# Optimization experiments

Measured on AMD Instinct MI355X. Metric: run time of the kernel, lower is better.

The kernel has to match this reference:

```python
import jax, jax.numpy as jnp
import numpy as np

N_NODES = 50000
N_EDGES = 800000
IN_DIM = 128
HID = 64
ZDIM = 64
N_GRAPHS = 64


def gcn_conv(x, W, b, src, dst, n):
    # PyG GCNConv: add self-loops, symmetric deg^-1/2 normalization,
    # linear transform then gather-scatter aggregation.
    h = x @ W  # [N, out]
    loops = jnp.arange(n, dtype=src.dtype)
    s = jnp.concatenate([src, loops])
    d = jnp.concatenate([dst, loops])
    deg = jnp.zeros((n,), h.dtype).at[d].add(1.0)  # includes self-loops -> >=1
    dinv = jax.lax.rsqrt(deg)
    norm = dinv[s] * dinv[d]  # [E+N]
    msg = h[s] * norm[:, None]  # gather [E+N, out]
    out = jnp.zeros_like(h).at[d].add(msg)  # scatter-add
    return out + b


def mean_pool(h, batch, num_graphs):
    sums = jax.ops.segment_sum(h, batch, num_segments=num_graphs)
    cnt = jax.ops.segment_sum(jnp.ones((h.shape[0],), h.dtype), batch,
                              num_segments=num_graphs)
    return sums / jnp.maximum(cnt, 1.0)[:, None]


def setup_inputs() -> dict:
    key = jax.random.key(0)
    ks = jax.random.split(key, 9)
    x = jax.random.normal(ks[0], (N_NODES, IN_DIM), jnp.float32)
    edge_index = jax.random.randint(ks[1], (2, N_EDGES), 0, N_NODES, jnp.int64 if jax.config.jax_enable_x64 else jnp.int32)
    batch = jnp.sort(jax.random.randint(ks[2], (N_NODES,), 0, N_GRAPHS))
    s1 = 1.0 / np.sqrt(IN_DIM)
    s2 = 1.0 / np.sqrt(HID)
    W1 = jax.random.uniform(ks[3], (IN_DIM, HID), jnp.float32, -s1, s1)
    b1 = jnp.zeros((HID,), jnp.float32)
    Wmu = jax.random.uniform(ks[4], (HID, ZDIM), jnp.float32, -s2, s2)
    bmu = jnp.zeros((ZDIM,), jnp.float32)
    Wsig = jax.random.uniform(ks[5], (HID, ZDIM), jnp.float32, -s2, s2)
    bsig = jnp.zeros((ZDIM,), jnp.float32)
    return {"x": x, "edge_index": edge_index, "batch": batch,
            "num_graphs": N_GRAPHS, "W1": W1, "b1": b1,
            "Wmu": Wmu, "bmu": bmu, "Wsig": Wsig, "bsig": bsig}


def reference(x, edge_index, batch, num_graphs, W1, b1, Wmu, bmu, Wsig, bsig):
    src, dst = edge_index[0], edge_index[1]
    n = x.shape[0]
    h = jax.nn.elu(gcn_conv(x, W1, b1, src, dst, n))
    z_mu = mean_pool(jax.nn.elu(gcn_conv(h, Wmu, bmu, src, dst, n)), batch, num_graphs)
    z_sigma = mean_pool(jax.nn.elu(gcn_conv(h, Wsig, bsig, src, dst, n)), batch, num_graphs)
    return (z_mu, z_sigma)
```

## Files before the change

kernel.cpp:

```cpp
#include <hip/hip_runtime.h>
#include <hip/hip_fp16.h>


#define IN_DIM 128
#define HID 64
#define ZDIM 64
#define N_GRAPHS 64
#define SCAN_B 1024

typedef _Float16 half8 __attribute__((ext_vector_type(8)));
typedef float f32x4 __attribute__((ext_vector_type(4)));

__device__ __forceinline__ float elu1(float x) {
    return x > 0.f ? x : expm1f(x);
}

#define ACC8(RV, MV) do { \
    const __half2* _hp = (const __half2*)&(RV); \
    float2 _f0 = __half22float2(_hp[0]); \
    float2 _f1 = __half22float2(_hp[1]); \
    float2 _f2 = __half22float2(_hp[2]); \
    float2 _f3 = __half22float2(_hp[3]); \
    acc[0] = fmaf((MV), _f0.x, acc[0]); \
    acc[1] = fmaf((MV), _f0.y, acc[1]); \
    acc[2] = fmaf((MV), _f1.x, acc[2]); \
    acc[3] = fmaf((MV), _f1.y, acc[3]); \
    acc[4] = fmaf((MV), _f2.x, acc[4]); \
    acc[5] = fmaf((MV), _f2.y, acc[5]); \
    acc[6] = fmaf((MV), _f3.x, acc[6]); \
    acc[7] = fmaf((MV), _f3.y, acc[7]); \
  } while (0)

__global__ __launch_bounds__(256) void k_count_wfrag(const int* __restrict__ dst,
                                                     int* __restrict__ kc,
                                                     int* __restrict__ rank, int E,
                                                     const float* __restrict__ W1,
                                                     const float* __restrict__ Wmu,
                                                     const float* __restrict__ Wsig,
                                                     __half* __restrict__ F1,
                                                     __half* __restrict__ Fmu,
                                                     __half* __restrict__ Fsig,
                                                     int cntBlocks) {
    if ((int)blockIdx.x < cntBlocks) {
        int e = (blockIdx.x * 256 + threadIdx.x) * 2;
        if (e + 1 < E) {
            int2 d2 = *(const int2*)&dst[e];
            int r0 = atomicAdd(&kc[d2.x], 1);
            int r1 = atomicAdd(&kc[d2.y], 1);
            *(int2*)&rank[e] = make_int2(r0, r1);
        } else if (e < E) {
            rank[e] = atomicAdd(&kc[dst[e]], 1);
        }
        return;
    }
    int e = (blockIdx.x - cntBlocks) * 256 + threadIdx.x;
    if (e < 8192) {
        int j = e & 7, l = (e >> 3) & 63, ct = (e >> 9) & 3, ks = e >> 11;
        F1[e] = __float2half(W1[(ks * 32 + ((l >> 4) & 3) * 8 + j) * 64 + ct * 16 + (l & 15)]);
    }
    if (e < 4096) {
        int j = e & 7, l = (e >> 3) & 63, ct = (e >> 9) & 3, ks = e >> 11;
        int widx = (ks * 32 + ((l >> 4) & 3) * 8 + j) * 64 + ct * 16 + (l & 15);
        Fmu[e] = __float2half(Wmu[widx]);
        Fsig[e] = __float2half(Wsig[widx]);
    }
}

__global__ __launch_bounds__(SCAN_B) void k_scan1(const int* __restrict__ kc,
                                                  int* __restrict__ bsum, int n) {
    __shared__ int wpart[16];
    int tid = threadIdx.x, lane = tid & 63, w = tid >> 6;
    int i = blockIdx.x * SCAN_B + tid;
    int v = (i < n) ? kc[i] : 0;
#pragma unroll
    for (int d = 1; d < 64; d <<= 1) v += __shfl_xor(v, d, 64);
    if (lane == 0) wpart[w] = v;
    __syncthreads();
    if (tid < 16) {
        int t = wpart[tid];
#pragma unroll
        for (int d = 1; d < 16; d <<= 1) t += __shfl_xor(t, d, 64);
        if (tid == 0) bsum[blockIdx.x] = t;
    }
}

__global__ __launch_bounds__(SCAN_B) void k_scan3(const int* __restrict__ kc,
                                                  const int* __restrict__ bsum,
                                                  int* __restrict__ offs,
                                                  float* __restrict__ dinv,
                                                  int n, int nb) {
    __shared__ int wsum[16];
    __shared__ int sbase;
    int tid = threadIdx.x, lane = tid & 63, w = tid >> 6;
    if (tid < 64) {
        int v = (tid < nb) ? bsum[tid] : 0;
        int s = v;
#pragma unroll
        for (int d = 1; d < 64; d <<= 1) {
            int u = __shfl_up(s, d, 64);
            if (tid >= d) s += u;
        }
        if (tid == blockIdx.x) sbase = s - v;
    }
    int i = blockIdx.x * SCAN_B + tid;
    int v = (i < n) ? kc[i] : 0;
    int s = v;
#pragma unroll
    for (int d = 1; d < 64; d <<= 1) {
        int u = __shfl_up(s, d, 64);
        if (lane >= d) s += u;
    }
    if (lane == 63) wsum[w] = s;
    __syncthreads();
    if (tid < 16) {
        int t = wsum[tid];
#pragma unroll
        for (int d = 1; d < 16; d <<= 1) {
            int u = __shfl_up(t, d, 64);
            if (tid >= d) t += u;
        }
        wsum[tid] = t;
    }
    __syncthreads();
    int base = sbase + ((w == 0) ? 0 : wsum[w - 1]);
    if (i < n) {
        offs[i + 1] = base + s;
        dinv[i] = 1.0f / sqrtf(1.0f + (float)v);
        if (i == 0) offs[0] = 0;
    }
}

__global__ __launch_bounds__(256) void k_fill_mm1(const int* __restrict__ src,
                                                  const int* __restrict__ dst,
                                                  const int* __restrict__ rank,
                                                  const int* __restrict__ offs,
                                                  int* __restrict__ csr, int E,
                                                  const float* __restrict__ x,
                                                  const __half* __restrict__ F1,
                                                  const float* __restrict__ dinv,
                                                  __half* __restrict__ ts1h, int n,
                                                  int fillBlocks) {
    if ((int)blockIdx.x < fillBlocks) {
        int e = (blockIdx.x * 256 + threadIdx.x) * 2;
        if (e + 1 < E) {
            int2 s2 = *(const int2*)&src[e];
            int2 d2 = *(const int2*)&dst[e];
            int2 r2 = *(const int2*)&rank[e];
            csr[offs[d2.x] + r2.x] = s2.x;
            csr[offs[d2.y] + r2.y] = s2.y;
        } else if (e < E) {
            csr[offs[dst[e]] + rank[e]] = src[e];
        }
        return;
    }
    int bid = blockIdx.x - fillBlocks;
    int l = threadIdx.x & 63;
    int wave = threadIdx.x >> 6;
    int m0 = bid * 64 + wave * 16;
    int row_a = m0 + (l & 15);
    if (row_a >= n) row_a = n - 1;
    int kg = l >> 4;

    f32x4 acc0 = {0.f, 0.f, 0.f, 0.f};
    f32x4 acc1 = acc0, acc2 = acc0, acc3 = acc0;

    const float* xr = x + (size_t)row_a * IN_DIM + kg * 8;
#pragma unroll
    for (int ks = 0; ks < 4; ++ks) {
        float4 xa = *(const float4*)(xr + ks * 32);
        float4 xb = *(const float4*)(xr + ks * 32 + 4);
        half8 a;
        a[0] = (_Float16)xa.x; a[1] = (_Float16)xa.y;
        a[2] = (_Float16)xa.z; a[3] = (_Float16)xa.w;
        a[4] = (_Float16)xb.x; a[5] = (_Float16)xb.y;
        a[6] = (_Float16)xb.z; a[7] = (_Float16)xb.w;
        const __half* fb = F1 + ((size_t)(ks * 4) * 64 + l) * 8;
        half8 b0 = *(const half8*)(fb);
        half8 b1 = *(const half8*)(fb + 512);
        half8 b2 = *(const half8*)(fb + 1024);
        half8 b3 = *(const half8*)(fb + 1536);
        acc0 = __builtin_amdgcn_mfma_f32_16x16x32_f16(a, b0, acc0, 0, 0, 0);
        acc1 = __builtin_amdgcn_mfma_f32_16x16x32_f16(a, b1, acc1, 0, 0, 0);
        acc2 = __builtin_amdgcn_mfma_f32_16x16x32_f16(a, b2, acc2, 0, 0, 0);
        acc3 = __builtin_amdgcn_mfma_f32_16x16x32_f16(a, b3, acc3, 0, 0, 0);
    }
    int col = l & 15;
#pragma unroll
    for (int r = 0; r < 4; ++r) {
        int row = m0 + kg * 4 + r;
        if (row < n) {
            float di = dinv[row];
            __half* p = &ts1h[(size_t)row * 64 + col];
            p[0]  = __float2half(acc0[r] * di);
            p[16] = __float2half(acc1[r] * di);
            p[32] = __float2half(acc2[r] * di);
            p[48] = __float2half(acc3[r] * di);
        }
    }
}

__global__ __launch_bounds__(256) void k_gather_hh(const int* __restrict__ off,
                                                   const int* __restrict__ csr,
                                                   const float* __restrict__ dinv,
                                                   const __half* __restrict__ ts,
                                                   const float* __restrict__ b1,
                                                   __half* __restrict__ hh, int n) {
    int node = blockIdx.x * 4 + (threadIdx.x >> 6);
    if (node >= n) return;
    int lane = threadIdx.x & 63;
    int g = lane >> 3, sub = lane & 7;
    int s0 = off[node], s1 = off[node + 1];
    float acc[8];
#pragma unroll
    for (int j = 0; j < 8; ++j) acc[j] = 0.f;

    if (s1 > s0) {
        int last = s1 - 1;
        int p0 = s0 + g, p1 = p0 + 8, p2 = p0 + 16, p3 = p0 + 24;
        int i0 = csr[p0 < s1 ? p0 : last];
        int i1 = csr[p1 < s1 ? p1 : last];
        int i2 = csr[p2 < s1 ? p2 : last];
        int i3 = csr[p3 < s1 ? p3 : last];
        float4 r0 = *(const float4*)&ts[(size_t)i0 * 64 + sub * 8];
        float4 r1 = *(const float4*)&ts[(size_t)i1 * 64 + sub * 8];
        float4 r2 = *(const float4*)&ts[(size_t)i2 * 64 + sub * 8];
        float4 r3 = *(const float4*)&ts[(size_t)i3 * 64 + sub * 8];
        float m0 = (p0 < s1) ? 1.f : 0.f;
        float m1 = (p1 < s1) ? 1.f : 0.f;
        float m2 = (p2 < s1) ? 1.f : 0.f;
        float m3 = (p3 < s1) ? 1.f : 0.f;
        ACC8(r0, m0);
        ACC8(r1, m1);
        ACC8(r2, m2);
        ACC8(r3, m3);
        for (int k = s0 + 32 + g; k < s1; k += 8) {
            int iv = csr[k];
            float4 rv = *(const float4*)&ts[(size_t)iv * 64 + sub * 8];
            ACC8(rv, 1.f);
        }
    }

#pragma unroll
    for (int j = 0; j < 8; ++j) {
        acc[j] += __shfl_xor(acc[j], 8, 64);
        acc[j] += __shfl_xor(acc[j], 16, 64);
        acc[j] += __shfl_xor(acc[j], 32, 64);
    }

    if (g == 0) {
        float4 sr = *(const float4*)&ts[(size_t)node * 64 + sub * 8];
        const __half2* sh = (const __half2*)&sr;
        float di = dinv[node];
        const float4* b4 = (const float4*)b1;
        float4 ba = b4[sub * 2], bb = b4[sub * 2 + 1];
        float2 f0 = __half22float2(sh[0]);
        float2 f1 = __half22float2(sh[1]);
        float2 f2 = __half22float2(sh[2]);
        float2 f3 = __half22float2(sh[3]);
        float e0 = elu1((acc[0] + f0.x) * di + ba.x) * di;
        float e1 = elu1((acc[1] + f0.y) * di + ba.y) * di;
        float e2 = elu1((acc[2] + f1.x) * di + ba.z) * di;
        float e3 = elu1((acc[3] + f1.y) * di + ba.w) * di;
        float e4 = elu1((acc[4] + f2.x) * di + bb.x) * di;
        float e5 = elu1((acc[5] + f2.y) * di + bb.y) * di;
        float e6 = elu1((acc[6] + f3.x) * di + bb.z) * di;
        float e7 = elu1((acc[7] + f3.y) * di + bb.w) * di;
        float4 outv;
        __half2* op = (__half2*)&outv;
        op[0] = __floats2half2_rn(e0, e1);
        op[1] = __floats2half2_rn(e2, e3);
        op[2] = __floats2half2_rn(e4, e5);
        op[3] = __floats2half2_rn(e6, e7);
        *(float4*)&hh[(size_t)node * 64 + sub * 8] = outv;
    }
}

__global__ __launch_bounds__(256) void k_gather_g(const int* __restrict__ off,
                                                  const int* __restrict__ csr,
                                                  const float* __restrict__ dinv,
                                                  const __half* __restrict__ hh,
                                                  __half* __restrict__ gh2, int n) {
    int node = blockIdx.x * 4 + (threadIdx.x >> 6);
    if (node >= n) return;
    int lane = threadIdx.x & 63;
    int g = lane >> 3, sub = lane & 7;
    int s0 = off[node], s1 = off[node + 1];
    float acc[8];
#pragma unroll
    for (int j = 0; j < 8; ++j) acc[j] = 0.f;

    if (s1 > s0) {
        int last = s1 - 1;
        int p0 = s0 + g, p1 = p0 + 8, p2 = p0 + 16, p3 = p0 + 24;
        int i0 = csr[p0 < s1 ? p0 : last];
        int i1 = csr[p1 < s1 ? p1 : last];
        int i2 = csr[p2 < s1 ? p2 : last];
        int i3 = csr[p3 < s1 ? p3 : last];
        float4 r0 = *(const float4*)&hh[(size_t)i0 * 64 + sub * 8];
        float4 r1 = *(const float4*)&hh[(size_t)i1 * 64 + sub * 8];
        float4 r2 = *(const float4*)&hh[(size_t)i2 * 64 + sub * 8];
        float4 r3 = *(const float4*)&hh[(size_t)i3 * 64 + sub * 8];
        float m0 = (p0 < s1) ? 1.f : 0.f;
        float m1 = (p1 < s1) ? 1.f : 0.f;
        float m2 = (p2 < s1) ? 1.f : 0.f;
        float m3 = (p3 < s1) ? 1.f : 0.f;
        ACC8(r0, m0);
        ACC8(r1, m1);
        ACC8(r2, m2);
        ACC8(r3, m3);
        for (int k = s0 + 32 + g; k < s1; k += 8) {
            int iv = csr[k];
            float4 rv = *(const float4*)&hh[(size_t)iv * 64 + sub * 8];
            ACC8(rv, 1.f);
        }
    }

#pragma unroll
    for (int j = 0; j < 8; ++j) {
        acc[j] += __shfl_xor(acc[j], 8, 64);
        acc[j] += __shfl_xor(acc[j], 16, 64);
        acc[j] += __shfl_xor(acc[j], 32, 64);
    }

    if (g == 0) {
        float4 sr = *(const float4*)&hh[(size_t)node * 64 + sub * 8];
        const __half2* sh = (const __half2*)&sr;
        float di = dinv[node];
        float2 f0 = __half22float2(sh[0]);
        float2 f1 = __half22float2(sh[1]);
        float2 f2 = __half22float2(sh[2]);
        float2 f3 = __half22float2(sh[3]);
        float4 outv;
        __half2* op = (__half2*)&outv;
        op[0] = __floats2half2_rn((acc[0] + f0.x) * di, (acc[1] + f0.y) * di);
        op[1] = __floats2half2_rn((acc[2] + f1.x) * di, (acc[3] + f1.y) * di);
        op[2] = __floats2half2_rn((acc[4] + f2.x) * di, (acc[5] + f2.y) * di);
        op[3] = __floats2half2_rn((acc[6] + f3.x) * di, (acc[7] + f3.y) * di);
        *(float4*)&gh2[(size_t)node * 64 + sub * 8] = outv;
    }
}

__global__ __launch_bounds__(256) void k_mm_pool(const __half* __restrict__ gh2,
                                                 const __half* __restrict__ Fmu,
                                                 const __half* __restrict__ Fsig,
                                                 const float* __restrict__ bmu,
                                                 const float* __restrict__ bsig,
                                                 const int* __restrict__ batch,
                                                 float* __restrict__ sums, int n) {
    __shared__ float wc[64 * 132];
    __shared__ int bs[64];
    const int tid = threadIdx.x;
    int l = tid & 63, wave = tid >> 6;
    int m0 = blockIdx.x * 64;
    int row_a = m0 + wave * 16 + (l & 15);
    if (row_a >= n) row_a = n - 1;
    int kg = l >> 4;

    f32x4 am[4], as[4];
#pragma unroll
    for (int ct = 0; ct < 4; ++ct) {
        am[ct] = (f32x4){0.f, 0.f, 0.f, 0.f};
        as[ct] = (f32x4){0.f, 0.f, 0.f, 0.f};
    }

    const __half* gr = gh2 + (size_t)row_a * 64 + kg * 8;
#pragma unroll
    for (int ks = 0; ks < 2; ++ks) {
        half8 a = *(const half8*)(gr + ks * 32);
        const __half* fm = Fmu + ((size_t)(ks * 4) * 64 + l) * 8;
        const __half* fs = Fsig + ((size_t)(ks * 4) * 64 + l) * 8;
#pragma unroll
        for (int ct = 0; ct < 4; ++ct) {
            half8 bm = *(const half8*)(fm + ct * 512);
            half8 bv = *(const half8*)(fs + ct * 512);
            am[ct] = __builtin_amdgcn_mfma_f32_16x16x32_f16(a, bm, am[ct], 0, 0, 0);
            as[ct] = __builtin_amdgcn_mfma_f32_16x16x32_f16(a, bv, as[ct], 0, 0, 0);
        }
    }

    if (tid < 64) bs[tid] = (m0 + tid < n) ? batch[m0 + tid] : -1;

    int col = l & 15;
#pragma unroll
    for (int ct = 0; ct < 4; ++ct) {
        float bM = bmu[ct * 16 + col];
        float bS = bsig[ct * 16 + col];
#pragma unroll
        for (int r = 0; r < 4; ++r) {
            int rr = wave * 16 + kg * 4 + r;
            wc[rr * 132 + ct * 16 + col] = elu1(am[ct][r] + bM);
            wc[rr * 132 + 64 + ct * 16 + col] = elu1(as[ct][r] + bS);
        }
    }
    __syncthreads();

    int d = tid & 127, seg = tid >> 7;
    int base = (d < 64) ? d : (64 * 64 - 64 + d);
    float acc = 0.f;
    int gcur = -1;
    int r0 = seg * 32;
    for (int r = r0; r < r0 + 32; ++r) {
        int gb = bs[r];
        if (gb < 0) break;
        float v = wc[r * 132 + d];
        if (gb != gcur) {
            if (gcur >= 0) atomicAdd(&sums[base + gcur * 64], acc);
            acc = 0.f;
            gcur = gb;
        }
        acc += v;
    }
    if (gcur >= 0) atomicAdd(&sums[base + gcur * 64], acc);
}

__global__ void k_pool_final(const float* __restrict__ sums,
                             const int* __restrict__ batch,
                             float* __restrict__ out, int n) {
    int i = blockIdx.x * blockDim.x + threadIdx.x;
    if (i >= 2 * N_GRAPHS * ZDIM) return;
    int g = (i >> 6) & 63;
    int lo = 0, hi = n;
    while (lo < hi) { int m = (lo + hi) >> 1; if (batch[m] < g) lo = m + 1; else hi = m; }
    int s = lo;
    lo = s; hi = n;
    while (lo < hi) { int m = (lo + hi) >> 1; if (batch[m] < g + 1) lo = m + 1; else hi = m; }
    float c = fmaxf((float)(lo - s), 1.0f);
    out[i] = sums[i] / c;
}

extern "C" void kernel_launch(void* const* d_in, const int* in_sizes, int n_in,
                              void* d_out, int out_size, void* d_ws, size_t ws_size,
                              hipStream_t stream) {
    const float* x    = (const float*)d_in[0];
    const int*   ei   = (const int*)d_in[1];
    const int*   batch= (const int*)d_in[2];
    const float* W1   = (const float*)d_in[4];
    const float* b1   = (const float*)d_in[5];
    const float* Wmu  = (const float*)d_in[6];
    const float* bmu  = (const float*)d_in[7];
    const float* Wsig = (const float*)d_in[8];
    const float* bsig = (const float*)d_in[9];
    float* out = (float*)d_out;

    const int n = in_sizes[0] / IN_DIM;
    const int E = in_sizes[1] / 2;
    const int* src = ei;
    const int* dst = ei + E;
    const int NSB = (n + SCAN_B - 1) / SCAN_B;

    float* ws = (float*)d_ws;
    size_t off_w = 0;
    int*   kc   = (int*)(ws + off_w); off_w += 50048;
    float* sums = ws + off_w; off_w += 8192;
    float* dinv = ws + off_w; off_w += 50048;
    int*   offs = (int*)(ws + off_w); off_w += 50056;
    int*   bsum = (int*)(ws + off_w); off_w += 64;
    int*   rank = (int*)(ws + off_w); off_w += 800000;
    int*   csr  = (int*)(ws + off_w); off_w += 800000;
    off_w = (off_w + 15) & ~(size_t)15;
    __half* F1   = (__half*)(ws + off_w); off_w += 4096;
    __half* Fmu  = (__half*)(ws + off_w); off_w += 2048;
    __half* Fsig = (__half*)(ws + off_w); off_w += 2048;
    const size_t BIG = (size_t)n * 64;
    __half* ts1h = (__half*)(ws + off_w); off_w += BIG / 2;
    __half* hh   = (__half*)(ws + off_w); off_w += BIG / 2;
    __half* gh2  = (__half*)(ws + off_w); off_w += BIG / 2;

    const int gE2 = (E + 511) / 512;
    const int gNW = (n + 3) / 4;
    const int NB  = (n + 63) / 64;

    hipMemsetAsync(kc, 0, (50048 + 8192) * sizeof(int), stream);
    k_count_wfrag<<<gE2 + 32, 256, 0, stream>>>(dst, kc, rank, E,
                                                W1, Wmu, Wsig, F1, Fmu, Fsig, gE2);
    k_scan1<<<NSB, SCAN_B, 0, stream>>>(kc, bsum, n);
    k_scan3<<<NSB, SCAN_B, 0, stream>>>(kc, bsum, offs, dinv, n, NSB);

    k_fill_mm1<<<gE2 + NB, 256, 0, stream>>>(src, dst, rank, offs, csr, E,
                                             x, F1, dinv, ts1h, n, gE2);

    k_gather_hh<<<gNW, 256, 0, stream>>>(offs, csr, dinv, ts1h, b1, hh, n);

    k_gather_g<<<gNW, 256, 0, stream>>>(offs, csr, dinv, hh, gh2, n);

    k_mm_pool<<<NB, 256, 0, stream>>>(gh2, Fmu, Fsig, bmu, bsig, batch, sums, n);
    k_pool_final<<<(2 * N_GRAPHS * ZDIM + 255) / 256, 256, 0, stream>>>(sums, batch, out, n);
}
```

Before: 216.0 us.

## Split node features into two 32-column halves for cache-friendly gathers

The layer-1 output and hidden features are stored as two separate half-width arrays (columns 0-31 and 32-63). The gather kernels process one half per block, two nodes per wave. Block indices interleave halves in groups of four so concurrent blocks work on the same half. Each gather pass then touches a 3.2 MB working set instead of 6.4 MB, which should raise L2/LLC hit rates for the random neighbor reads. The cost is that CSR indices and offsets are read twice, the grid doubles, and each gathered row segment is only 64 bytes.

```diff
diff --git a/kernel.cpp b/kernel.cpp
--- a/kernel.cpp
+++ b/kernel.cpp
@@ -138,7 +138,8 @@
                                                   const float* __restrict__ x,
                                                   const __half* __restrict__ F1,
                                                   const float* __restrict__ dinv,
-                                                  __half* __restrict__ ts1h, int n,
+                                                  __half* __restrict__ tsA,
+                                                  __half* __restrict__ tsB, int n,
                                                   int fillBlocks) {
     if ((int)blockIdx.x < fillBlocks) {
         int e = (blockIdx.x * 256 + threadIdx.x) * 2;
@@ -190,11 +191,12 @@
         int row = m0 + kg * 4 + r;
         if (row < n) {
             float di = dinv[row];
-            __half* p = &ts1h[(size_t)row * 64 + col];
-            p[0]  = __float2half(acc0[r] * di);
-            p[16] = __float2half(acc1[r] * di);
-            p[32] = __float2half(acc2[r] * di);
-            p[48] = __float2half(acc3[r] * di);
+            __half* pA = &tsA[(size_t)row * 32 + col];
+            pA[0]  = __float2half(acc0[r] * di);
+            pA[16] = __float2half(acc1[r] * di);
+            __half* pB = &tsB[(size_t)row * 32 + col];
+            pB[0]  = __float2half(acc2[r] * di);
+            pB[16] = __float2half(acc3[r] * di);
         }
     }
 }
@@ -202,14 +204,26 @@
 __global__ __launch_bounds__(256) void k_gather_hh(const int* __restrict__ off,
                                                    const int* __restrict__ csr,
                                                    const float* __restrict__ dinv,
-                                                   const __half* __restrict__ ts,
+                                                   const __half* __restrict__ tsA,
+                                                   const __half* __restrict__ tsB,
                                                    const float* __restrict__ b1,
-                                                   __half* __restrict__ hh, int n) {
-    int node = blockIdx.x * 4 + (threadIdx.x >> 6);
-    if (node >= n) return;
+                                                   __half* __restrict__ hhA,
+                                                   __half* __restrict__ hhB, int n) {
+    int bid = blockIdx.x;
+    int half = (bid >> 2) & 1;
+    int jb = (bid >> 3) * 4 + (bid & 3);
+    int wv = threadIdx.x >> 6;
+    int node0 = jb * 8 + wv * 2;
+    if (node0 >= n) return;
+    const __half* T = half ? tsB : tsA;
+    __half* H = half ? hhB : hhA;
     int lane = threadIdx.x & 63;
-    int g = lane >> 3, sub = lane & 7;
-    int s0 = off[node], s1 = off[node + 1];
+    int nsel = lane >> 5;
+    int node = node0 + nsel;
+    bool valid = node < n;
+    int nodec = valid ? node : n - 1;
+    int l32 = lane & 31, g = l32 >> 2, sub = l32 & 3;
+    int s0 = off[nodec], s1 = off[nodec + 1];
     float acc[8];
 #pragma unroll
     for (int j = 0; j < 8; ++j) acc[j] = 0.f;
@@ -221,10 +235,10 @@
         int i1 = csr[p1 < s1 ? p1 : last];
         int i2 = csr[p2 < s1 ? p2 : last];
         int i3 = csr[p3 < s1 ? p3 : last];
-        float4 r0 = *(const float4*)&ts[(size_t)i0 * 64 + sub * 8];
-        float4 r1 = *(const float4*)&ts[(size_t)i1 * 64 + sub * 8];
-        float4 r2 = *(const float4*)&ts[(size_t)i2 * 64 + sub * 8];
-        float4 r3 = *(const float4*)&ts[(size_t)i3 * 64 + sub * 8];
+        float4 r0 = *(const float4*)&T[(size_t)i0 * 32 + sub * 8];
+        float4 r1 = *(const float4*)&T[(size_t)i1 * 32 + sub * 8];
+        float4 r2 = *(const float4*)&T[(size_t)i2 * 32 + sub * 8];
+        float4 r3 = *(const float4*)&T[(size_t)i3 * 32 + sub * 8];
         float m0 = (p0 < s1) ? 1.f : 0.f;
         float m1 = (p1 < s1) ? 1.f : 0.f;
         float m2 = (p2 < s1) ? 1.f : 0.f;
@@ -235,56 +249,68 @@
         ACC8(r3, m3);
         for (int k = s0 + 32 + g; k < s1; k += 8) {
             int iv = csr[k];
-            float4 rv = *(const float4*)&ts[(size_t)iv * 64 + sub * 8];
+            float4 rv = *(const float4*)&T[(size_t)iv * 32 + sub * 8];
             ACC8(rv, 1.f);
         }
     }
 
 #pragma unroll
     for (int j = 0; j < 8; ++j) {
+        acc[j] += __shfl_xor(acc[j], 4, 64);
         acc[j] += __shfl_xor(acc[j], 8, 64);
         acc[j] += __shfl_xor(acc[j], 16, 64);
-        acc[j] += __shfl_xor(acc[j], 32, 64);
-    }
-
-    if (g == 0) {
-        float4 sr = *(const float4*)&ts[(size_t)node * 64 + sub * 8];
+    }
+
+    if (g == 0 && valid) {
+        int e0 = sub * 8;
+        float4 sr = *(const float4*)&T[(size_t)nodec * 32 + e0];
         const __half2* sh = (const __half2*)&sr;
-        float di = dinv[node];
-        const float4* b4 = (const float4*)b1;
-        float4 ba = b4[sub * 2], bb = b4[sub * 2 + 1];
+        float di = dinv[nodec];
+        const float* bh = b1 + half * 32 + e0;
+        float4 ba = *(const float4*)bh;
+        float4 bb = *(const float4*)(bh + 4);
         float2 f0 = __half22float2(sh[0]);
         float2 f1 = __half22float2(sh[1]);
         float2 f2 = __half22float2(sh[2]);
         float2 f3 = __half22float2(sh[3]);
-        float e0 = elu1((acc[0] + f0.x) * di + ba.x) * di;
-        float e1 = elu1((acc[1] + f0.y) * di + ba.y) * di;
-        float e2 = elu1((acc[2] + f1.x) * di + ba.z) * di;
-        float e3 = elu1((acc[3] + f1.y) * di + ba.w) * di;
-        float e4 = elu1((acc[4] + f2.x) * di + bb.x) * di;
-        float e5 = elu1((acc[5] + f2.y) * di + bb.y) * di;
-        float e6 = elu1((acc[6] + f3.x) * di + bb.z) * di;
-        float e7 = elu1((acc[7] + f3.y) * di + bb.w) * di;
+        float e0v = elu1((acc[0] + f0.x) * di + ba.x) * di;
+        float e1v = elu1((acc[1] + f0.y) * di + ba.y) * di;
+        float e2v = elu1((acc[2] + f1.x) * di + ba.z) * di;
+        float e3v = elu1((acc[3] + f1.y) * di + ba.w) * di;
+        float e4v = elu1((acc[4] + f2.x) * di + bb.x) * di;
+        float e5v = elu1((acc[5] + f2.y) * di + bb.y) * di;
+        float e6v = elu1((acc[6] + f3.x) * di + bb.z) * di;
+        float e7v = elu1((acc[7] + f3.y) * di + bb.w) * di;
         float4 outv;
         __half2* op = (__half2*)&outv;
-        op[0] = __floats2half2_rn(e0, e1);
-        op[1] = __floats2half2_rn(e2, e3);
-        op[2] = __floats2half2_rn(e4, e5);
-        op[3] = __floats2half2_rn(e6, e7);
-        *(float4*)&hh[(size_t)node * 64 + sub * 8] = outv;
+        op[0] = __floats2half2_rn(e0v, e1v);
+        op[1] = __floats2half2_rn(e2v, e3v);
+        op[2] = __floats2half2_rn(e4v, e5v);
+        op[3] = __floats2half2_rn(e6v, e7v);
+        *(float4*)&H[(size_t)node * 32 + e0] = outv;
     }
 }
 
 __global__ __launch_bounds__(256) void k_gather_g(const int* __restrict__ off,
                                                   const int* __restrict__ csr,
                                                   const float* __restrict__ dinv,
-                                                  const __half* __restrict__ hh,
+                                                  const __half* __restrict__ hhA,
+                                                  const __half* __restrict__ hhB,
                                                   __half* __restrict__ gh2, int n) {
-    int node = blockIdx.x * 4 + (threadIdx.x >> 6);
-    if (node >= n) return;
+    int bid = blockIdx.x;
+    int half = (bid >> 2) & 1;
+    int jb = (bid >> 3) * 4 + (bid & 3);
+    int wv = threadIdx.x >> 6;
+    int node0 = jb * 8 + wv * 2;
+    if (node0 >= n) return;
+    const __half* T = half ? hhB : hhA;
     int lane = threadIdx.x & 63;
-    int g = lane >> 3, sub = lane & 7;
-    int s0 = off[node], s1 = off[node + 1];
+    int nsel = lane >> 5;
+    int node = node0 + nsel;
+    bool valid = node < n;
+    int nodec = valid ? node : n - 1;
+    int l32 = lane & 31, g = l32 >> 2, sub = l32 & 3;
+    int s0 = off[nodec], s1 = off[nodec + 1];
     float acc[8];
 #pragma unroll
     for (int j = 0; j < 8; ++j) acc[j] = 0.f;
@@ -296,10 +322,10 @@
         int i1 = csr[p1 < s1 ? p1 : last];
         int i2 = csr[p2 < s1 ? p2 : last];
         int i3 = csr[p3 < s1 ? p3 : last];
-        float4 r0 = *(const float4*)&hh[(size_t)i0 * 64 + sub * 8];
-        float4 r1 = *(const float4*)&hh[(size_t)i1 * 64 + sub * 8];
-        float4 r2 = *(const float4*)&hh[(size_t)i2 * 64 + sub * 8];
-        float4 r3 = *(const float4*)&hh[(size_t)i3 * 64 + sub * 8];
+        float4 r0 = *(const float4*)&T[(size_t)i0 * 32 + sub * 8];
+        float4 r1 = *(const float4*)&T[(size_t)i1 * 32 + sub * 8];
+        float4 r2 = *(const float4*)&T[(size_t)i2 * 32 + sub * 8];
+        float4 r3 = *(const float4*)&T[(size_t)i3 * 32 + sub * 8];
         float m0 = (p0 < s1) ? 1.f : 0.f;
         float m1 = (p1 < s1) ? 1.f : 0.f;
         float m2 = (p2 < s1) ? 1.f : 0.f;
@@ -310,22 +336,23 @@
         ACC8(r3, m3);
         for (int k = s0 + 32 + g; k < s1; k += 8) {
             int iv = csr[k];
-            float4 rv = *(const float4*)&hh[(size_t)iv * 64 + sub * 8];
+            float4 rv = *(const float4*)&T[(size_t)iv * 32 + sub * 8];
             ACC8(rv, 1.f);
         }
     }
 
 #pragma unroll
     for (int j = 0; j < 8; ++j) {
+        acc[j] += __shfl_xor(acc[j], 4, 64);
         acc[j] += __shfl_xor(acc[j], 8, 64);
         acc[j] += __shfl_xor(acc[j], 16, 64);
-        acc[j] += __shfl_xor(acc[j], 32, 64);
-    }
-
-    if (g == 0) {
-        float4 sr = *(const float4*)&hh[(size_t)node * 64 + sub * 8];
+    }
+
+    if (g == 0 && valid) {
+        int e0 = sub * 8;
+        float4 sr = *(const float4*)&T[(size_t)nodec * 32 + e0];
         const __half2* sh = (const __half2*)&sr;
-        float di = dinv[node];
+        float di = dinv[nodec];
         float2 f0 = __half22float2(sh[0]);
         float2 f1 = __half22float2(sh[1]);
         float2 f2 = __half22float2(sh[2]);
@@ -336,7 +363,7 @@
         op[1] = __floats2half2_rn((acc[2] + f1.x) * di, (acc[3] + f1.y) * di);
         op[2] = __floats2half2_rn((acc[4] + f2.x) * di, (acc[5] + f2.y) * di);
         op[3] = __floats2half2_rn((acc[6] + f3.x) * di, (acc[7] + f3.y) * di);
-        *(float4*)&gh2[(size_t)node * 64 + sub * 8] = outv;
+        *(float4*)&gh2[(size_t)node * 64 + half * 32 + e0] = outv;
     }
 }
 
@@ -461,14 +488,18 @@
     __half* F1   = (__half*)(ws + off_w); off_w += 4096;
     __half* Fmu  = (__half*)(ws + off_w); off_w += 2048;
     __half* Fsig = (__half*)(ws + off_w); off_w += 2048;
-    const size_t BIG = (size_t)n * 64;
-    __half* ts1h = (__half*)(ws + off_w); off_w += BIG / 2;
-    __half* hh   = (__half*)(ws + off_w); off_w += BIG / 2;
-    __half* gh2  = (__half*)(ws + off_w); off_w += BIG / 2;
+    const size_t HALFF = (size_t)50048 * 16;
+    __half* tsA = (__half*)(ws + off_w); off_w += HALFF;
+    __half* tsB = (__half*)(ws + off_w); off_w += HALFF;
+    __half* hhA = (__half*)(ws + off_w); off_w += HALFF;
+    __half* hhB = (__half*)(ws + off_w); off_w += HALFF;
+    __half* gh2 = (__half*)(ws + off_w); off_w += (size_t)50048 * 32;
 
     const int gE2 = (E + 511) / 512;
-    const int gNW = (n + 3) / 4;
     const int NB  = (n + 63) / 64;
+    const int bph = (n + 7) / 8;
+    const int bph4 = (bph + 3) & ~3;
+    const int gG = 2 * bph4;
 
     hipMemsetAsync(kc, 0, (50048 + 8192) * sizeof(int), stream);
     k_count_wfrag<<<gE2 + 32, 256, 0, stream>>>(dst, kc, rank, E,
@@ -477,11 +508,11 @@
     k_scan3<<<NSB, SCAN_B, 0, stream>>>(kc, bsum, offs, dinv, n, NSB);
 
     k_fill_mm1<<<gE2 + NB, 256, 0, stream>>>(src, dst, rank, offs, csr, E,
-                                             x, F1, dinv, ts1h, n, gE2);
-
-    k_gather_hh<<<gNW, 256, 0, stream>>>(offs, csr, dinv, ts1h, b1, hh, n);
-
-    k_gather_g<<<gNW, 256, 0, stream>>>(offs, csr, dinv, hh, gh2, n);
+                                             x, F1, dinv, tsA, tsB, n, gE2);
+
+    k_gather_hh<<<gG, 256, 0, stream>>>(offs, csr, dinv, tsA, tsB, b1, hhA, hhB, n);
+
+    k_gather_g<<<gG, 256, 0, stream>>>(offs, csr, dinv, hhA, hhB, gh2, n);
 
     k_mm_pool<<<NB, 256, 0, stream>>>(gh2, Fmu, Fsig, bmu, bsig, batch, sums, n);
     k_pool_final<<<(2 * N_GRAPHS * ZDIM + 255) / 256, 256, 0, stream>>>(sums, batch, out, n);
```

Measured after the change: 214.1 us, median of 2. Within noise of the previous version (-0.9%).
